# Kernel tuning notes

Hardware: AMD Instinct MI355X
Metric: run time of the kernel (lower is better)

Reference implementation:

```python
import jax, jax.numpy as jnp
import numpy as np


def _pool_mat(n_in, n_out):
    # AdaptiveAvgPool1d(n_out) over a length-n_in axis, as a dense [n_out, n_in] averaging matrix.
    M = np.zeros((n_out, n_in), dtype=np.float32)
    for i in range(n_out):
        s = (i * n_in) // n_out
        e = -(-((i + 1) * n_in) // n_out)  # ceil
        M[i, s:e] = 1.0 / (e - s)
    return M


def _ln(x, g, b, eps=1e-5):
    m = jnp.mean(x, axis=-1, keepdims=True)
    xc = x - m
    v = jnp.mean(xc * xc, axis=-1, keepdims=True)
    return xc * jax.lax.rsqrt(v + eps) * g + b


def setup_inputs():
    T, TOK, P, N, D, L, C = 16, 16384, 8192, 32768, 128, 8, 16
    key = jax.random.key(0)
    ks = jax.random.split(key, 9)
    x = jax.random.normal(ks[0], (T, TOK, D), dtype=jnp.float32)
    # P node-token positions per timestamp (models padded_node_mask with P True entries)
    node_pos = jnp.sort(jax.vmap(lambda k: jax.random.permutation(k, TOK)[:P])(jax.random.split(ks[1], T)), axis=1).astype(jnp.int32)
    # unique entire-graph node ids per timestamp (scatter destinations)
    node_ids = jax.vmap(lambda k: jax.random.permutation(k, N)[:P])(jax.random.split(ks[2], T)).astype(jnp.int32)
    g_enc = 1.0 + 0.1 * jax.random.normal(ks[3], (D,), dtype=jnp.float32)
    b_enc = 0.1 * jax.random.normal(ks[4], (D,), dtype=jnp.float32)
    g_fin = 1.0 + 0.1 * jax.random.normal(ks[5], (L * C,), dtype=jnp.float32)
    b_fin = 0.1 * jax.random.normal(ks[6], (L * C,), dtype=jnp.float32)
    g_dec = 1.0 + 0.1 * jax.random.normal(ks[7], (C,), dtype=jnp.float32)
    b_dec = 0.1 * jax.random.normal(ks[8], (C,), dtype=jnp.float32)
    return {"x": x, "g_enc": g_enc, "b_enc": b_enc, "g_fin": g_fin, "b_fin": b_fin,
            "g_dec": g_dec, "b_dec": b_dec, "node_pos": node_pos, "node_ids": node_ids,
            "num_nodes": N}


def reference(x, g_enc, b_enc, g_fin, b_fin, g_dec, b_dec, node_pos, node_ids, num_nodes):
    T, TOK, D = x.shape
    C = g_dec.shape[0]
    L = g_fin.shape[0] // C
    N = int(num_nodes)
    # ---- encode ----
    xn = _ln(x, g_enc, b_enc)                                   # encode_layer_norm
    nodes = jnp.take_along_axis(xn, node_pos[:, :, None], axis=1)  # masked gather [T,P,D]
    # _to_entire: scatter node embeddings into zero [T,N,D]
    tee = jnp.zeros((T, N, D), x.dtype).at[jnp.arange(T)[:, None], node_ids].set(nodes)
    A1 = jnp.asarray(_pool_mat(D, C))                            # AdaptiveAvgPool1d(comp_dim)
    pooled = jnp.einsum('tnd,cd->tnc', tee, A1)                  # [T,N,C]
    groups = np.array_split(np.arange(N), L)
    max_len = max(len(g) for g in groups)
    stacked = np.stack([np.pad(g, (0, max_len - len(g))) for g in groups])  # [L,max_len]
    grouped = jnp.take(pooled, jnp.asarray(stacked), axis=1)     # [T,L,max_len,C]
    comp = (grouped.sum(axis=2) / max_len).reshape(T, 1, L * C)  # segment mean-pool
    comp = _ln(comp, g_fin, b_fin)                               # encode_final_layer_norm
    # ---- decode ----
    vals = jnp.broadcast_to(comp.reshape(T, L, 1, C), (T, L, max_len, C)).reshape(T, L * max_len, C)
    tee2 = jnp.zeros((T, N, C), x.dtype).at[:, jnp.asarray(stacked.reshape(-1)), :].set(vals)
    dn = _ln(tee2, g_dec, b_dec)                                 # decode_norm
    A2 = jnp.asarray(_pool_mat(C, D))                            # AdaptiveAvgPool1d(embed_dim)
    out = jnp.einsum('tnc,dc->tnd', dn, A2)                      # [T,N,D]
    return out
```

## Files before the change

### kernel.cpp

```cpp
#include <hip/hip_runtime.h>

#define T_   16
#define TOK_ 16384
#define P_   8192
#define N_   32768
#define D_   128
#define L_   8
#define C_   16

typedef float f32x2 __attribute__((ext_vector_type(2)));
typedef float f32x4 __attribute__((ext_vector_type(4)));

constexpr int K1_BLOCKS     = 1024;
constexpr int BLOCKS_PER_T  = 64;
constexpr int ROWS_PER_WAVE = 32;

__global__ __launch_bounds__(256) void k1_gather_ln_pool(
    const float* __restrict__ x,
    const float* __restrict__ g_enc, const float* __restrict__ b_enc,
    const int* __restrict__ node_pos, const int* __restrict__ node_ids,
    float* __restrict__ partial)
{
    __shared__ float lds[4 * 128];
    const int tid   = threadIdx.x;
    const int lane  = tid & 63;
    const int wid   = tid >> 6;
    const int b     = blockIdx.x;
    const int t     = b >> 6;
    const int chunk = b & 63;
    const int pbase = chunk * 128 + wid * ROWS_PER_WAVE;
    const int tP    = t * P_;
    const float* xt = x + (size_t)t * TOK_ * D_ + 2 * lane;

    const float ge0 = g_enc[2 * lane], ge1 = g_enc[2 * lane + 1];
    const float be0 = b_enc[2 * lane], be1 = b_enc[2 * lane + 1];

    const int posv = node_pos[tP + pbase + (lane & 31)];
    const int nidv = node_ids[tP + pbase + (lane & 31)];

    float acc[L_];
#pragma unroll
    for (int ll = 0; ll < L_; ++ll) acc[ll] = 0.f;

    f32x2 b0, b1, b2, b3;
    {
        int p0 = __shfl(posv, 0), p1 = __shfl(posv, 1);
        int p2 = __shfl(posv, 2), p3 = __shfl(posv, 3);
        b0 = __builtin_nontemporal_load((const f32x2*)(xt + (size_t)p0 * D_));
        b1 = __builtin_nontemporal_load((const f32x2*)(xt + (size_t)p1 * D_));
        b2 = __builtin_nontemporal_load((const f32x2*)(xt + (size_t)p2 * D_));
        b3 = __builtin_nontemporal_load((const f32x2*)(xt + (size_t)p3 * D_));
    }

#pragma unroll
    for (int g = 0; g < ROWS_PER_WAVE / 4; ++g) {
        f32x2 c0 = b0, c1 = b1, c2 = b2, c3 = b3;
        if (g < ROWS_PER_WAVE / 4 - 1) {
            const int rb = (g + 1) * 4;
            int p0 = __shfl(posv, rb + 0), p1 = __shfl(posv, rb + 1);
            int p2 = __shfl(posv, rb + 2), p3 = __shfl(posv, rb + 3);
            b0 = __builtin_nontemporal_load((const f32x2*)(xt + (size_t)p0 * D_));
            b1 = __builtin_nontemporal_load((const f32x2*)(xt + (size_t)p1 * D_));
            b2 = __builtin_nontemporal_load((const f32x2*)(xt + (size_t)p2 * D_));
            b3 = __builtin_nontemporal_load((const f32x2*)(xt + (size_t)p3 * D_));
        }
        float s0 = c0.x + c0.y, q0 = c0.x * c0.x + c0.y * c0.y;
        float s1 = c1.x + c1.y, q1 = c1.x * c1.x + c1.y * c1.y;
        float s2 = c2.x + c2.y, q2 = c2.x * c2.x + c2.y * c2.y;
        float s3 = c3.x + c3.y, q3 = c3.x * c3.x + c3.y * c3.y;
#pragma unroll
        for (int m = 1; m < 64; m <<= 1) {
            s0 += __shfl_xor(s0, m); q0 += __shfl_xor(q0, m);
            s1 += __shfl_xor(s1, m); q1 += __shfl_xor(q1, m);
            s2 += __shfl_xor(s2, m); q2 += __shfl_xor(q2, m);
            s3 += __shfl_xor(s3, m); q3 += __shfl_xor(q3, m);
        }
#pragma unroll
        for (int k = 0; k < 4; ++k) {
            const f32x2 v = (k == 0) ? c0 : (k == 1) ? c1 : (k == 2) ? c2 : c3;
            const float s = (k == 0) ? s0 : (k == 1) ? s1 : (k == 2) ? s2 : s3;
            const float q = (k == 0) ? q0 : (k == 1) ? q1 : (k == 2) ? q2 : q3;
            const float mean = s * (1.f / 128.f);
            const float rstd = rsqrtf(q * (1.f / 128.f) - mean * mean + 1e-5f);
            const float srow = (v.x - mean) * rstd * ge0 + be0
                             + (v.y - mean) * rstd * ge1 + be1;
            const int l = __shfl(nidv, g * 4 + k) >> 12;
#pragma unroll
            for (int ll = 0; ll < L_; ++ll) acc[ll] += (ll == l) ? srow : 0.f;
        }
    }

#pragma unroll
    for (int ll = 0; ll < L_; ++ll) {
        acc[ll] += __shfl_xor(acc[ll], 1);
        acc[ll] += __shfl_xor(acc[ll], 2);
    }
    const int c = lane >> 2;
    if ((lane & 3) == 0) {
#pragma unroll
        for (int ll = 0; ll < L_; ++ll) lds[wid * 128 + ll * 16 + c] = acc[ll];
    }
    __syncthreads();
    if (tid < 128) {
        const float sum = lds[tid] + lds[128 + tid] + lds[256 + tid] + lds[384 + tid];
        partial[(size_t)b * 128 + tid] = sum;
    }
}

__global__ __launch_bounds__(64) void k2_finalize(
    const float* __restrict__ partial,
    const float* __restrict__ g_fin, const float* __restrict__ b_fin,
    const float* __restrict__ g_dec, const float* __restrict__ b_dec,
    float* __restrict__ decoded)
{
    const int t = blockIdx.x;
    const int lane = threadIdx.x;
    const float* pb = partial + (size_t)t * BLOCKS_PER_T * 128;
    float a0 = 0.f, a1 = 0.f;
#pragma unroll 8
    for (int k = 0; k < BLOCKS_PER_T; ++k) {
        a0 += pb[k * 128 + lane];
        a1 += pb[k * 128 + 64 + lane];
    }
    a0 *= (1.f / 32768.f);
    a1 *= (1.f / 32768.f);

    float s = a0 + a1, ss = a0 * a0 + a1 * a1;
#pragma unroll
    for (int m = 1; m < 64; m <<= 1) {
        s  += __shfl_xor(s, m);
        ss += __shfl_xor(ss, m);
    }
    const float mean = s * (1.f / 128.f);
    const float rstd = rsqrtf(ss * (1.f / 128.f) - mean * mean + 1e-5f);
    const float c0 = (a0 - mean) * rstd * g_fin[lane]      + b_fin[lane];
    const float c1 = (a1 - mean) * rstd * g_fin[lane + 64] + b_fin[lane + 64];

    float s0 = c0, q0 = c0 * c0, s1 = c1, q1 = c1 * c1;
#pragma unroll
    for (int m = 1; m < 16; m <<= 1) {
        s0 += __shfl_xor(s0, m); q0 += __shfl_xor(q0, m);
        s1 += __shfl_xor(s1, m); q1 += __shfl_xor(q1, m);
    }
    const float m0 = s0 * (1.f / 16.f), m1 = s1 * (1.f / 16.f);
    const float r0 = rsqrtf(q0 * (1.f / 16.f) - m0 * m0 + 1e-5f);
    const float r1 = rsqrtf(q1 * (1.f / 16.f) - m1 * m1 + 1e-5f);
    const int c = lane & 15;
    const float gd = g_dec[c], bd = b_dec[c];
    decoded[t * 128 + lane]      = (c0 - m0) * r0 * gd + bd;
    decoded[t * 128 + 64 + lane] = (c1 - m1) * r1 * gd + bd;
}

__global__ __launch_bounds__(256) void k3_broadcast(
    const float* __restrict__ decoded, f32x4* __restrict__ out)
{
    const int tid   = threadIdx.x;
    const int b     = blockIdx.x;
    const int t     = b >> 7;
    const int chunk = b & 127;
    const int l     = chunk >> 4;
    const float val = decoded[(t << 7) + (l << 4) + ((tid & 31) >> 1)];
    const f32x4 v4 = {val, val, val, val};
    f32x4* p = out + (((size_t)t << 20) + ((size_t)chunk << 13) + tid);
#pragma unroll
    for (int it = 0; it < 32; ++it)
        __builtin_nontemporal_store(v4, p + (it << 8));
}

extern "C" void kernel_launch(void* const* d_in, const int* in_sizes, int n_in,
                              void* d_out, int out_size, void* d_ws, size_t ws_size,
                              hipStream_t stream)
{
    const float* x      = (const float*)d_in[0];
    const float* g_enc  = (const float*)d_in[1];
    const float* b_enc  = (const float*)d_in[2];
    const float* g_fin  = (const float*)d_in[3];
    const float* b_fin  = (const float*)d_in[4];
    const float* g_dec  = (const float*)d_in[5];
    const float* b_dec  = (const float*)d_in[6];
    const int*   node_pos = (const int*)d_in[7];
    const int*   node_ids = (const int*)d_in[8];

    float* partial = (float*)d_ws;
    float* decoded = partial + (size_t)K1_BLOCKS * 128;
    float* out = (float*)d_out;

    hipLaunchKernelGGL(k1_gather_ln_pool, dim3(K1_BLOCKS), dim3(256), 0, stream,
                       x, g_enc, b_enc, node_pos, node_ids, partial);
    hipLaunchKernelGGL(k2_finalize, dim3(T_), dim3(64), 0, stream,
                       partial, g_fin, b_fin, g_dec, b_dec, decoded);
    hipLaunchKernelGGL(k3_broadcast, dim3(2048), dim3(256), 0, stream,
                       decoded, (f32x4*)out);
}
```

Baseline: 82.74 us.

## Restructure gather-LN-pool: 16 lanes per row, 4 rows per wave-load, folded affine

Each wave now handles four rows at once, with 16 lanes per row and each lane loading 8 contiguous floats (two float4 loads), instead of the whole wave loading one row as float2. The layer-norm affine and the pooling sum are folded algebraically into a dot product with gamma plus precomputed sums of gamma and beta. This shortens the shuffle reductions to 16 lanes and issues all loads up front. The grid doubles to 2048 blocks with 16 rows per wave, which means more partials for k2 to reduce. Nontemporal loads are dropped.

```diff
diff --git a/kernel.cpp b/kernel.cpp
--- a/kernel.cpp
+++ b/kernel.cpp
@@ -11,9 +11,9 @@
 typedef float f32x2 __attribute__((ext_vector_type(2)));
 typedef float f32x4 __attribute__((ext_vector_type(4)));
 
-constexpr int K1_BLOCKS     = 1024;
-constexpr int BLOCKS_PER_T  = 64;
-constexpr int ROWS_PER_WAVE = 32;
+constexpr int K1_BLOCKS     = 2048;
+constexpr int BLOCKS_PER_T  = 128;
+constexpr int ROWS_PER_WAVE = 16;
 
 __global__ __launch_bounds__(256) void k1_gather_ln_pool(
     const float* __restrict__ x,
@@ -25,80 +25,67 @@
     const int tid   = threadIdx.x;
     const int lane  = tid & 63;
     const int wid   = tid >> 6;
+    const int j     = lane & 15;
+    const int q     = lane >> 4;
     const int b     = blockIdx.x;
-    const int t     = b >> 6;
-    const int chunk = b & 63;
-    const int pbase = chunk * 128 + wid * ROWS_PER_WAVE;
+    const int t     = b >> 7;
+    const int chunk = b & 127;
+    const int pbase = chunk * 64 + wid * ROWS_PER_WAVE;
     const int tP    = t * P_;
-    const float* xt = x + (size_t)t * TOK_ * D_ + 2 * lane;
+    const float* xt = x + (size_t)t * TOK_ * D_;
 
-    const float ge0 = g_enc[2 * lane], ge1 = g_enc[2 * lane + 1];
-    const float be0 = b_enc[2 * lane], be1 = b_enc[2 * lane + 1];
+    const f32x4 g0 = *(const f32x4*)(g_enc + 8 * j);
+    const f32x4 g1 = *(const f32x4*)(g_enc + 8 * j + 4);
+    const f32x4 bb0 = *(const f32x4*)(b_enc + 8 * j);
+    const f32x4 bb1 = *(const f32x4*)(b_enc + 8 * j + 4);
+    const float G = g0.x + g0.y + g0.z + g0.w + g1.x + g1.y + g1.z + g1.w;
+    const float B = bb0.x + bb0.y + bb0.z + bb0.w + bb1.x + bb1.y + bb1.z + bb1.w;
 
-    const int posv = node_pos[tP + pbase + (lane & 31)];
-    const int nidv = node_ids[tP + pbase + (lane & 31)];
+    const int posv = node_pos[tP + pbase + j];
+    const int nidv = node_ids[tP + pbase + j];
+
+    f32x4 va[4], vb[4];
+#pragma unroll
+    for (int i = 0; i < 4; ++i) {
+        const int p = __shfl(posv, i * 4 + q);
+        const float* row = xt + (size_t)p * D_ + 8 * j;
+        va[i] = *(const f32x4*)(row);
+        vb[i] = *(const f32x4*)(row + 4);
+    }
 
     float acc[L_];
 #pragma unroll
     for (int ll = 0; ll < L_; ++ll) acc[ll] = 0.f;
 
-    f32x2 b0, b1, b2, b3;
-    {
-        int p0 = __shfl(posv, 0), p1 = __shfl(posv, 1);
-        int p2 = __shfl(posv, 2), p3 = __shfl(posv, 3);
-        b0 = __builtin_nontemporal_load((const f32x2*)(xt + (size_t)p0 * D_));
-        b1 = __builtin_nontemporal_load((const f32x2*)(xt + (size_t)p1 * D_));
-        b2 = __builtin_nontemporal_load((const f32x2*)(xt + (size_t)p2 * D_));
-        b3 = __builtin_nontemporal_load((const f32x2*)(xt + (size_t)p3 * D_));
-    }
-
 #pragma unroll
-    for (int g = 0; g < ROWS_PER_WAVE / 4; ++g) {
-        f32x2 c0 = b0, c1 = b1, c2 = b2, c3 = b3;
-        if (g < ROWS_PER_WAVE / 4 - 1) {
-            const int rb = (g + 1) * 4;
-            int p0 = __shfl(posv, rb + 0), p1 = __shfl(posv, rb + 1);
-            int p2 = __shfl(posv, rb + 2), p3 = __shfl(posv, rb + 3);
-            b0 = __builtin_nontemporal_load((const f32x2*)(xt + (size_t)p0 * D_));
-            b1 = __builtin_nontemporal_load((const f32x2*)(xt + (size_t)p1 * D_));
-            b2 = __builtin_nontemporal_load((const f32x2*)(xt + (size_t)p2 * D_));
-            b3 = __builtin_nontemporal_load((const f32x2*)(xt + (size_t)p3 * D_));
+    for (int i = 0; i < 4; ++i) {
+        const f32x4 a = va[i], c = vb[i];
+        float s  = a.x + a.y + a.z + a.w + c.x + c.y + c.z + c.w;
+        float ss = a.x*a.x + a.y*a.y + a.z*a.z + a.w*a.w
+                 + c.x*c.x + c.y*c.y + c.z*c.z + c.w*c.w;
+        float dot = a.x*g0.x + a.y*g0.y + a.z*g0.z + a.w*g0.w
+                  + c.x*g1.x + c.y*g1.y + c.z*g1.z + c.w*g1.w;
+#pragma unroll
+        for (int m = 1; m < 16; m <<= 1) {
+            s  += __shfl_xor(s, m);
+            ss += __shfl_xor(ss, m);
         }
-        float s0 = c0.x + c0.y, q0 = c0.x * c0.x + c0.y * c0.y;
-        float s1 = c1.x + c1.y, q1 = c1.x * c1.x + c1.y * c1.y;
-        float s2 = c2.x + c2.y, q2 = c2.x * c2.x + c2.y * c2.y;
-        float s3 = c3.x + c3.y, q3 = c3.x * c3.x + c3.y * c3.y;
+        const float mean = s * (1.f / 128.f);
+        const float rstd = rsqrtf(ss * (1.f / 128.f) - mean * mean + 1e-5f);
+        const float srow = (dot - mean * G) * rstd + B;
+        const int l = __shfl(nidv, i * 4 + q) >> 12;
 #pragma unroll
-        for (int m = 1; m < 64; m <<= 1) {
-            s0 += __shfl_xor(s0, m); q0 += __shfl_xor(q0, m);
-            s1 += __shfl_xor(s1, m); q1 += __shfl_xor(q1, m);
-            s2 += __shfl_xor(s2, m); q2 += __shfl_xor(q2, m);
-            s3 += __shfl_xor(s3, m); q3 += __shfl_xor(q3, m);
-        }
-#pragma unroll
-        for (int k = 0; k < 4; ++k) {
-            const f32x2 v = (k == 0) ? c0 : (k == 1) ? c1 : (k == 2) ? c2 : c3;
-            const float s = (k == 0) ? s0 : (k == 1) ? s1 : (k == 2) ? s2 : s3;
-            const float q = (k == 0) ? q0 : (k == 1) ? q1 : (k == 2) ? q2 : q3;
-            const float mean = s * (1.f / 128.f);
-            const float rstd = rsqrtf(q * (1.f / 128.f) - mean * mean + 1e-5f);
-            const float srow = (v.x - mean) * rstd * ge0 + be0
-                             + (v.y - mean) * rstd * ge1 + be1;
-            const int l = __shfl(nidv, g * 4 + k) >> 12;
-#pragma unroll
-            for (int ll = 0; ll < L_; ++ll) acc[ll] += (ll == l) ? srow : 0.f;
-        }
+        for (int ll = 0; ll < L_; ++ll) acc[ll] += (ll == l) ? srow : 0.f;
     }
 
 #pragma unroll
     for (int ll = 0; ll < L_; ++ll) {
-        acc[ll] += __shfl_xor(acc[ll], 1);
-        acc[ll] += __shfl_xor(acc[ll], 2);
+        acc[ll] += __shfl_xor(acc[ll], 16);
+        acc[ll] += __shfl_xor(acc[ll], 32);
     }
-    const int c = lane >> 2;
-    if ((lane & 3) == 0) {
+    if (lane < 16) {
 #pragma unroll
-        for (int ll = 0; ll < L_; ++ll) lds[wid * 128 + ll * 16 + c] = acc[ll];
+        for (int ll = 0; ll < L_; ++ll) lds[wid * 128 + ll * 16 + j] = acc[ll];
     }
     __syncthreads();
     if (tid < 128) {
```

Measured after the change: 72.69 us. 1.14x faster.
